# Optimization experiments

Hardware: AMD Instinct MI355X
Metric: run time of the kernel (lower is better)

The kernel has to match this reference:

```python
import jax, jax.numpy as jnp
from jax import lax
import numpy as np

B, N, P, NB = 64, 16, 20, 30      # frames, boxes/frame, num_persons, num_behaviors
C, F, OUT, SR = 1024, 14, 3, 2    # fmap channels, fmap size, roi output, sampling ratio
EPS = 1e-5


def roi_align_one(fmap, boxes):
    """fmap: [C,H,W]; boxes: [K,4]=(x1,y1,x2,y2) in fmap coords. Returns [K,C,OUT,OUT].
    torchvision-style roi_align (aligned=False) with fixed sampling_ratio=SR."""
    H, W = fmap.shape[1], fmap.shape[2]
    x1, y1, x2, y2 = boxes[:, 0], boxes[:, 1], boxes[:, 2], boxes[:, 3]
    rw = jnp.maximum(x2 - x1, 1.0)
    rh = jnp.maximum(y2 - y1, 1.0)
    S = OUT * SR
    pos = (jnp.arange(S, dtype=fmap.dtype) + 0.5) / SR            # sample pos in bin units
    ys = jnp.clip(y1[:, None] + pos[None, :] * (rh / OUT)[:, None], 0.0, H - 1.0)  # [K,S]
    xs = jnp.clip(x1[:, None] + pos[None, :] * (rw / OUT)[:, None], 0.0, W - 1.0)
    y0 = jnp.floor(ys); x0 = jnp.floor(xs)
    y0i = y0.astype(jnp.int32); x0i = x0.astype(jnp.int32)
    y1i = jnp.minimum(y0i + 1, H - 1); x1i = jnp.minimum(x0i + 1, W - 1)
    wy = ys - y0; wx = xs - x0                                     # [K,S]
    g = lambda yi, xi: fmap[:, yi[:, :, None], xi[:, None, :]]     # [C,K,S,S]
    v = (g(y0i, x0i) * ((1 - wy)[:, :, None] * (1 - wx)[:, None, :])
         + g(y0i, x1i) * ((1 - wy)[:, :, None] * wx[:, None, :])
         + g(y1i, x0i) * (wy[:, :, None] * (1 - wx)[:, None, :])
         + g(y1i, x1i) * (wy[:, :, None] * wx[:, None, :]))
    v = jnp.transpose(v, (1, 0, 2, 3))                             # [K,C,S,S]
    K = boxes.shape[0]
    return v.reshape(K, C, OUT, SR, OUT, SR).mean(axis=(3, 5))     # avg over samples


roi_align = jax.vmap(roi_align_one, in_axes=(0, 0))


def bn(x, g, b, m, v):
    s = (g / jnp.sqrt(v + EPS))[None, :, None, None]
    return x * s + (b - m * g / jnp.sqrt(v + EPS))[None, :, None, None]


def leaky(x):
    return jnp.where(x > 0, x, 0.1 * x)


def behavior_conv(x, w1, g1, b1, m1, v1, w2, g2, b2, m2, v2):
    dn = ('NCHW', 'OIHW', 'NCHW')
    x = lax.conv_general_dilated(x, w1, (1, 1), 'SAME', dimension_numbers=dn)
    x = leaky(bn(x, g1, b1, m1, v1))
    x = lax.conv_general_dilated(x, w2, (1, 1), 'SAME', dimension_numbers=dn)
    return leaky(bn(x, g2, b2, m2, v2))


def forward(fmap, boxes, conv1_w, bn1_g, bn1_b, bn1_m, bn1_v,
            conv2_w, bn2_g, bn2_b, bn2_m, bn2_v,
            conv1d_w, conv1d_b, fc1_w, fc1_b, fc2_w, fc2_b, person_idx):
    # --- global feature: ROI over the whole fmap per frame ---
    gbox = jnp.broadcast_to(jnp.array([[0.0, 0.0, F, F]], jnp.float32), (B, 1, 4))
    g_roi = roi_align(fmap, gbox).reshape(B, C, OUT, OUT)          # [B,1024,3,3]
    g_feat = behavior_conv(g_roi, conv1_w, bn1_g, bn1_b, bn1_m, bn1_v,
                           conv2_w, bn2_g, bn2_b, bn2_m, bn2_v)    # [B,256,3,3]
    g_feat = g_feat.reshape(B, 256 * OUT * OUT)                    # [B,2304]

    # --- per-box ROI features ---
    i_roi = roi_align(fmap, boxes).reshape(B * N, C, OUT, OUT)     # [B*N,1024,3,3]
    i_feat = behavior_conv(i_roi, conv1_w, bn1_g, bn1_b, bn1_m, bn1_v,
                           conv2_w, bn2_g, bn2_b, bn2_m, bn2_v)
    i_feat = i_feat.reshape(B, N, 256 * OUT * OUT)                 # [B,N,2304]

    # --- scatter-accumulate into behavior tensor [B,P,2304] ---
    behavior = jnp.broadcast_to(g_feat[:, None, :], (B, P, 2304))
    bidx = jnp.broadcast_to(jnp.arange(B)[:, None], (B, N))
    behavior = behavior.at[bidx, person_idx].add(i_feat)

    # --- temporal conv1d across the batch axis for every person slot ---
    x = jnp.transpose(behavior, (1, 2, 0))                         # [P,2304,B]
    x = lax.conv_general_dilated(x, conv1d_w, (1,), 'SAME',
                                 dimension_numbers=('NCH', 'OIH', 'NCH'))
    x = x + conv1d_b[None, :, None]                                # [P,2304,B]

    # --- gather each (frame, box)'s person feature at its frame and classify ---
    x = jnp.transpose(x, (2, 0, 1))                                # [B,P,2304]
    feats = jnp.take_along_axis(x, person_idx[:, :, None], axis=1) # [B,N,2304]
    h = jax.nn.relu(feats @ fc1_w + fc1_b)                         # dropout off (eval)
    return h @ fc2_w + fc2_b                                       # [B,N,NB]


def setup_inputs() -> dict:
    key = jax.random.key(0)
    ks = jax.random.split(key, 16)
    fmap = jax.random.normal(ks[0], (B, C, F, F), jnp.float32)
    lo = jax.random.uniform(ks[1], (B, N, 2), jnp.float32, 0.0, 9.0)
    sz = jax.random.uniform(ks[2], (B, N, 2), jnp.float32, 2.0, 5.0)
    hi = jnp.minimum(lo + sz, float(F))
    boxes = jnp.concatenate([lo, hi], axis=-1)                     # (x1,y1,x2,y2)
    person_idx = jax.random.randint(ks[3], (B, N), 0, P)
    s = lambda k, shape, fan: jax.random.normal(k, shape, jnp.float32) / np.sqrt(fan)
    return {
        'fmap': fmap, 'boxes': boxes, 'person_idx': person_idx,
        'conv1_w': s(ks[4], (512, 1024, 3, 3), 1024 * 9),
        'bn1_g': jnp.ones(512), 'bn1_b': jnp.zeros(512),
        'bn1_m': jnp.zeros(512), 'bn1_v': jnp.ones(512),
        'conv2_w': s(ks[5], (256, 512, 3, 3), 512 * 9),
        'bn2_g': jnp.ones(256), 'bn2_b': jnp.zeros(256),
        'bn2_m': jnp.zeros(256), 'bn2_v': jnp.ones(256),
        'conv1d_w': s(ks[6], (2304, 2304, 3), 2304 * 3),
        'conv1d_b': jnp.zeros(2304),
        'fc1_w': s(ks[7], (2304, 1024), 2304), 'fc1_b': jnp.zeros(1024),
        'fc2_w': s(ks[8], (1024, NB), 1024), 'fc2_b': jnp.zeros(NB),
    }


def reference(fmap, boxes, person_idx, conv1_w, bn1_g, bn1_b, bn1_m, bn1_v,
              conv2_w, bn2_g, bn2_b, bn2_m, bn2_v,
              conv1d_w, conv1d_b, fc1_w, fc1_b, fc2_w, fc2_b):
    return forward(fmap, boxes, conv1_w, bn1_g, bn1_b, bn1_m, bn1_v,
                   conv2_w, bn2_g, bn2_b, bn2_m, bn2_v,
                   conv1d_w, conv1d_b, fc1_w, fc1_b, fc2_w, fc2_b, person_idx)
```

## Files before the change

kernel.cpp:

```cpp
#include <hip/hip_runtime.h>
#include <hip/hip_bf16.h>
#include <cstdint>
#include <cstddef>

typedef __bf16 bf16;
typedef __bf16 bf16x8 __attribute__((ext_vector_type(8)));
typedef float f32x4 __attribute__((ext_vector_type(4)));

__device__ __forceinline__ void gload_lds16(const bf16* g, bf16* l) {
    __builtin_amdgcn_global_load_lds((const __attribute__((address_space(1))) void*)g,
                                     (__attribute__((address_space(3))) void*)l, 16, 0, 0);
}

template <int NT>
__global__ void __launch_bounds__(256) repack_w(const float* __restrict__ w, bf16* __restrict__ out,
                                                int OC, int IC) {
    int idx = blockIdx.x * 256 + threadIdx.x;
    if (idx >= OC * IC) return;
    int oc = idx / IC;
    int ic = idx - oc * IC;
    const float* src = w + (size_t)idx * NT;
    #pragma unroll
    for (int t = 0; t < NT; t++)
        out[(size_t)oc * NT * IC + t * IC + ic] = (bf16)src[t];
}

__global__ void __launch_bounds__(256) transpose_fc1(const float* __restrict__ w, bf16* __restrict__ out) {
    __shared__ float t[32][33];
    int iT = blockIdx.x * 32;
    int oT = blockIdx.y * 32;
    int tx = threadIdx.x, ty = threadIdx.y;
    #pragma unroll
    for (int j = 0; j < 4; j++)
        t[ty + j * 8][tx] = w[(size_t)(iT + ty + j * 8) * 1024 + oT + tx];
    __syncthreads();
    #pragma unroll
    for (int j = 0; j < 4; j++)
        out[(size_t)(oT + ty + j * 8) * 2304 + iT + tx] = (bf16)t[tx][ty + j * 8];
}

__global__ void __launch_bounds__(256) transpose_w2(const float* __restrict__ w, bf16* __restrict__ out) {
    int idx = blockIdx.x * 256 + threadIdx.x;
    if (idx >= 30 * 1024) return;
    int n = idx / 1024, k = idx - n * 1024;
    out[idx] = (bf16)w[(size_t)k * 30 + n];
}

__global__ void __launch_bounds__(256) setup_all(int* __restrict__ rb1t, int* __restrict__ rb2t,
                                                 int* __restrict__ rb1dt, int* __restrict__ rbfc,
                                                 const int* __restrict__ pidx,
                                                 bf16* __restrict__ zp1, bf16* __restrict__ zp2,
                                                 bf16* __restrict__ zp3,
                                                 const float* g1, const float* b1, const float* m1, const float* v1,
                                                 const float* g2, const float* b2, const float* m2, const float* v2,
                                                 float* __restrict__ s1, float* __restrict__ t1,
                                                 float* __restrict__ s2, float* __restrict__ t2) {
    int m = blockIdx.x * 256 + threadIdx.x;
    if (m < 9 * 9856) {
        int tap = m / 9856, r = m - tap * 9856;
        int mm = r < 9792 ? r : 0;
        int img = mm / 9, pos = mm - img * 9;
        int oy = pos / 3, ox = pos - oy * 3;
        int ty = tap / 3, tx = tap - ty * 3;
        int iy = oy + ty - 1, ix = ox + tx - 1;
        bool valid = (iy >= 0) & (iy < 3) & (ix >= 0) & (ix < 3);
        int cell = img * 9 + iy * 3 + ix;
        rb1t[m] = valid ? 1024 + cell * 1024 : 0;
        rb2t[m] = valid ? 512 + cell * 512 : 0;
    }
    if (m < 3 * 1280) {
        int tap = m / 1280, r = m - tap * 1280;
        int p = r >> 6, t = r & 63;
        int tt = t + tap - 1;
        bool valid = (tt >= 0) & (tt < 64);
        rb1dt[m] = valid ? 2304 + (p * 64 + tt) * 2304 : 0;
    }
    if (m < 1024) {
        int b = m >> 4;
        rbfc[m] = (b * 20 + pidx[m]) * 2304;
    }
    if (m < 1024) zp1[m] = (bf16)0.f;
    if (m < 512)  zp2[m] = (bf16)0.f;
    if (m < 2304) zp3[m] = (bf16)0.f;
    if (m < 512) {
        float sc = g1[m] * rsqrtf(v1[m] + 1e-5f);
        s1[m] = sc; t1[m] = b1[m] - m1[m] * sc;
    } else if (m < 768) {
        int i = m - 512;
        float sc = g2[i] * rsqrtf(v2[i] + 1e-5f);
        s2[i] = sc; t2[i] = b2[i] - m2[i] * sc;
    }
}

__global__ void __launch_bounds__(256) transpose_fmap(const float* __restrict__ fmap, bf16* __restrict__ fml) {
    __shared__ float t[32][33];
    int img = blockIdx.z;
    int hwT = blockIdx.x * 32;
    int cT  = blockIdx.y * 32;
    int tx = threadIdx.x, ty = threadIdx.y;
    #pragma unroll
    for (int j = 0; j < 4; j++) {
        int c = cT + ty + j * 8;
        int hw = hwT + tx;
        if (hw < 196)
            t[ty + j * 8][tx] = fmap[((size_t)img * 1024 + c) * 196 + hw];
    }
    __syncthreads();
    #pragma unroll
    for (int j = 0; j < 4; j++) {
        int hw = hwT + ty + j * 8;
        int c = cT + tx;
        if (hw < 196)
            fml[((size_t)img * 196 + hw) * 1024 + c] = (bf16)t[tx][ty + j * 8];
    }
}

__global__ void __launch_bounds__(128) roi_kernel2(const bf16* __restrict__ fml, const float* __restrict__ boxes,
                                                   bf16* __restrict__ a1c) {
    int box = blockIdx.x;
    int tid = threadIdx.x;
    float x1, y1, x2, y2;
    int img;
    if (box < 64) { img = box; x1 = 0.f; y1 = 0.f; x2 = 14.f; y2 = 14.f; }
    else {
        int ib = box - 64;
        img = ib >> 4;
        const float* bb = boxes + (size_t)ib * 4;
        x1 = bb[0]; y1 = bb[1]; x2 = bb[2]; y2 = bb[3];
    }
    float rw = fmaxf(x2 - x1, 1.f), rh = fmaxf(y2 - y1, 1.f);
    __shared__ float swy[6], swx[6];
    __shared__ int sy0[6], sx0[6];
    if (tid < 6) {
        int i = tid;
        float pos = ((float)i + 0.5f) * 0.5f;
        float yv = fminf(fmaxf(y1 + pos * (rh * (1.f / 3.f)), 0.f), 13.f);
        float y0 = floorf(yv);
        sy0[i] = (int)y0; swy[i] = yv - y0;
        float xv = fminf(fmaxf(x1 + pos * (rw * (1.f / 3.f)), 0.f), 13.f);
        float x0 = floorf(xv);
        sx0[i] = (int)x0; swx[i] = xv - x0;
    }
    __syncthreads();
    const bf16* base = fml + (size_t)img * 196 * 1024 + tid * 8;
    #pragma unroll
    for (int oy = 0; oy < 3; oy++) {
        #pragma unroll
        for (int ox = 0; ox < 3; ox++) {
            float acc[8];
            #pragma unroll
            for (int e = 0; e < 8; e++) acc[e] = 0.f;
            #pragma unroll
            for (int dy = 0; dy < 2; dy++) {
                int sy = 2 * oy + dy;
                int y0 = sy0[sy]; float wy = swy[sy];
                int y1i = min(y0 + 1, 13);
                #pragma unroll
                for (int dx = 0; dx < 2; dx++) {
                    int sx = 2 * ox + dx;
                    int x0 = sx0[sx]; float wx = swx[sx];
                    int x1i = min(x0 + 1, 13);
                    bf16x8 f00 = *(const bf16x8*)(base + (size_t)(y0 * 14 + x0) * 1024);
                    bf16x8 f01 = *(const bf16x8*)(base + (size_t)(y0 * 14 + x1i) * 1024);
                    bf16x8 f10 = *(const bf16x8*)(base + (size_t)(y1i * 14 + x0) * 1024);
                    bf16x8 f11 = *(const bf16x8*)(base + (size_t)(y1i * 14 + x1i) * 1024);
                    float w00 = (1.f - wy) * (1.f - wx), w01 = (1.f - wy) * wx;
                    float w10 = wy * (1.f - wx),         w11 = wy * wx;
                    #pragma unroll
                    for (int e = 0; e < 8; e++)
                        acc[e] += w00 * (float)f00[e] + w01 * (float)f01[e]
                                + w10 * (float)f10[e] + w11 * (float)f11[e];
                }
            }
            bf16x8 o;
            #pragma unroll
            for (int e = 0; e < 8; e++) o[e] = (bf16)(acc[e] * 0.25f);
            *(bf16x8*)(a1c + 1024 + ((size_t)box * 9 + oy * 3 + ox) * 1024 + tid * 8) = o;
        }
    }
}

__global__ void __launch_bounds__(256) assemble(const float* __restrict__ feat, const int* __restrict__ pidx,
                                                bf16* __restrict__ asm3) {
    int b = blockIdx.x;
    int p = blockIdx.y;
    __shared__ int idxs[16];
    if (threadIdx.x < 16) idxs[threadIdx.x] = pidx[b * 16 + threadIdx.x];
    __syncthreads();
    const float* g = feat + (size_t)b * 2304;
    for (int f = threadIdx.x; f < 2304; f += 256) {
        float v = g[f];
        #pragma unroll
        for (int n = 0; n < 16; n++)
            if (idxs[n] == p) v += feat[(size_t)(64 + b * 16 + n) * 2304 + f];
        asm3[2304 + ((size_t)p * 64 + b) * 2304 + f] = (bf16)v;
    }
}

template <int MODE, int NSPLIT>
__global__ void __launch_bounds__(256) gemm_k(const bf16* __restrict__ A, const int* __restrict__ rowtab,
                                              const bf16* __restrict__ Bw, float* __restrict__ outp) {
    constexpr int K   = MODE == 0 ? 9216 : MODE == 1 ? 4608 : MODE == 2 ? 6912 : 2304;
    constexpr int N   = MODE == 0 ? 512  : MODE == 1 ? 256  : MODE == 2 ? 2304 : 1024;
    constexpr int Cin = MODE == 0 ? 1024 : MODE == 1 ? 512  : 2304;
    constexpr int M   = MODE <= 1 ? 9792 : MODE == 2 ? 1280 : 1024;
    constexpr int MT  = MODE <= 1 ? 9856 : MODE == 2 ? 1280 : 1024;
    constexpr bool MPAD = (M % 128) != 0;
    constexpr int KTS = (K / 64) / NSPLIT;

    const int bm = blockIdx.y * 128;
    const int bn = blockIdx.x * 128;
    const int z  = blockIdx.z;
    const int tid = threadIdx.x;
    const int lane = tid & 63, wave = tid >> 6;
    const int q = lane >> 4, ln16 = lane & 15;
    const int wr = wave >> 1, wc = wave & 1;

    __shared__ __align__(16) bf16 As[128 * 64];
    __shared__ __align__(16) bf16 Bs[128 * 64];

    const int sr = lane >> 3;
    const int sc = ((lane & 7) ^ sr) * 8;
    const bf16* gB[4];
    #pragma unroll
    for (int u = 0; u < 4; u++)
        gB[u] = Bw + (size_t)(bn + wave * 32 + u * 8 + sr) * K + sc;

    f32x4 acc[4][4];
    #pragma unroll
    for (int mt = 0; mt < 4; mt++)
        #pragma unroll
        for (int nt = 0; nt < 4; nt++)
            acc[mt][nt] = (f32x4){0.f, 0.f, 0.f, 0.f};

    int rbA[4];
    int curtap = -1;
    for (int kt = z * KTS; kt < z * KTS + KTS; kt++) {
        const int k0 = kt * 64;
        const int tap = k0 / Cin;
        const int inner = k0 - tap * Cin;
        if (tap != curtap) {
            curtap = tap;
            #pragma unroll
            for (int u = 0; u < 4; u++)
                rbA[u] = rowtab[tap * MT + bm + wave * 32 + u * 8 + sr];
        }
        const int aoff = inner + sc;

        __syncthreads();
        #pragma unroll
        for (int u = 0; u < 4; u++)
            gload_lds16(A + (size_t)(rbA[u] + aoff), As + (wave * 32 + u * 8) * 64);
        #pragma unroll
        for (int u = 0; u < 4; u++)
            gload_lds16(gB[u] + k0, Bs + (wave * 32 + u * 8) * 64);
        __syncthreads();

        #pragma unroll
        for (int s = 0; s < 2; s++) {
            bf16x8 af[4], bfr[4];
            #pragma unroll
            for (int mt = 0; mt < 4; mt++) {
                int r = wr * 64 + mt * 16 + ln16;
                af[mt] = *(const bf16x8*)(As + r * 64 + (((4 * s + q) ^ (ln16 & 7)) << 3));
            }
            #pragma unroll
            for (int nt = 0; nt < 4; nt++) {
                int r = wc * 64 + nt * 16 + ln16;
                bfr[nt] = *(const bf16x8*)(Bs + r * 64 + (((4 * s + q) ^ (ln16 & 7)) << 3));
            }
            #pragma unroll
            for (int mt = 0; mt < 4; mt++)
                #pragma unroll
                for (int nt = 0; nt < 4; nt++)
                    acc[mt][nt] = __builtin_amdgcn_mfma_f32_16x16x32_bf16(af[mt], bfr[nt], acc[mt][nt], 0, 0, 0);
        }
    }

    #pragma unroll
    for (int mt = 0; mt < 4; mt++) {
        int gmBase = bm + wr * 64 + mt * 16 + q * 4;
        #pragma unroll
        for (int r = 0; r < 4; r++) {
            int gm = gmBase + r;
            if (MPAD && gm >= M) continue;
            #pragma unroll
            for (int nt = 0; nt < 4; nt++) {
                int gn = bn + wc * 64 + nt * 16 + ln16;
                outp[((size_t)z * M + gm) * N + gn] = acc[mt][nt][r];
            }
        }
    }
}

template <int RMODE>
__global__ void __launch_bounds__(256) reduce_k(const float* __restrict__ part, void* __restrict__ outp,
                                                const float* __restrict__ c0, const float* __restrict__ c1) {
    constexpr int M = RMODE == 0 ? 9792 : RMODE == 1 ? 1280 : RMODE == 2 ? 1024 : 9792;
    constexpr int N = RMODE == 0 ? 256  : RMODE == 1 ? 2304 : RMODE == 2 ? 1024 : 512;
    constexpr int S = RMODE == 0 ? 6    : RMODE == 1 ? 4    : RMODE == 2 ? 6    : 3;
    int idx = blockIdx.x * 256 + threadIdx.x;
    if (idx >= M * N) return;
    int m = idx / N, n = idx - m * N;
    float v = 0.f;
    #pragma unroll
    for (int s = 0; s < S; s++) v += part[(size_t)s * M * N + idx];
    if constexpr (RMODE == 0) {
        v = v * c0[n] + c1[n];
        v = v > 0.f ? v : 0.1f * v;
        int img = m / 9, pos = m - img * 9;
        ((float*)outp)[(size_t)img * 2304 + n * 9 + pos] = v;
    } else if constexpr (RMODE == 1) {
        v += c0[n];
        int p = m >> 6, t = m & 63;
        ((bf16*)outp)[((size_t)t * 20 + p) * 2304 + n] = (bf16)v;
    } else if constexpr (RMODE == 2) {
        v = fmaxf(v + c0[n], 0.f);
        ((bf16*)outp)[idx] = (bf16)v;
    } else {
        v = v * c0[n] + c1[n];
        v = v > 0.f ? v : 0.1f * v;
        ((bf16*)outp)[512 + (size_t)m * 512 + n] = (bf16)v;
    }
}

__global__ void __launch_bounds__(256) fc2_kernel(const bf16* __restrict__ h, const bf16* __restrict__ w2t,
                                                  const float* __restrict__ b2, float* __restrict__ out) {
    int tid = threadIdx.x;
    int m = blockIdx.x * 8 + (tid >> 5);
    int n = tid & 31;
    int n2 = n < 30 ? n : 29;
    const bf16* hr = h + (size_t)m * 1024;
    const bf16* wr = w2t + (size_t)n2 * 1024;
    float acc = 0.f;
    for (int k = 0; k < 1024; k += 8) {
        bf16x8 hv = *(const bf16x8*)(hr + k);
        bf16x8 wv = *(const bf16x8*)(wr + k);
        #pragma unroll
        for (int e = 0; e < 8; e++) acc += (float)hv[e] * (float)wv[e];
    }
    if (n < 30) out[(size_t)m * 30 + n] = acc + b2[n];
}

extern "C" void kernel_launch(void* const* d_in, const int* in_sizes, int n_in,
                              void* d_out, int out_size, void* d_ws, size_t ws_size,
                              hipStream_t stream) {
    const float* fmap     = (const float*)d_in[0];
    const float* boxes    = (const float*)d_in[1];
    const int*   pidx     = (const int*)d_in[2];
    const float* conv1_w  = (const float*)d_in[3];
    const float* bn1_g    = (const float*)d_in[4];
    const float* bn1_b    = (const float*)d_in[5];
    const float* bn1_m    = (const float*)d_in[6];
    const float* bn1_v    = (const float*)d_in[7];
    const float* conv2_w  = (const float*)d_in[8];
    const float* bn2_g    = (const float*)d_in[9];
    const float* bn2_b    = (const float*)d_in[10];
    const float* bn2_m    = (const float*)d_in[11];
    const float* bn2_v    = (const float*)d_in[12];
    const float* conv1d_w = (const float*)d_in[13];
    const float* conv1d_b = (const float*)d_in[14];
    const float* fc1_w    = (const float*)d_in[15];
    const float* fc1_b    = (const float*)d_in[16];
    const float* fc2_w    = (const float*)d_in[17];
    const float* fc2_b    = (const float*)d_in[18];
    float* out = (float*)d_out;

    char* ws = (char*)d_ws;

    float* s1    = (float*)(ws + 0);
    float* t1    = (float*)(ws + 2048);
    float* s2    = (float*)(ws + 4096);
    float* t2    = (float*)(ws + 5120);
    int*   rbfc  = (int*)(ws + 6144);
    int*   rb1dt = (int*)(ws + 10240);
    int*   rb1t  = (int*)(ws + 25600);
    int*   rb2t  = (int*)(ws + 380416);
    bf16*  fml    = (bf16*)(ws + 768000);
    float* part1  = (float*)(ws + 768000);
    float* part2  = (float*)(ws + 768000);
    float* part1d = (float*)(ws + 768000);
    float* partfc = (float*)(ws + 768000);
    bf16*  a1c    = (bf16*)(ws + 60930048);
    bf16*  wb1d   = (bf16*)(ws + 60930048);
    bf16*  fc1t   = (bf16*)(ws + 92780544);
    bf16*  xbuf   = (bf16*)(ws + 97499136);
    bf16*  hbuf   = (bf16*)(ws + 103397376);
    bf16*  w2t    = (bf16*)(ws + 105494528);
    bf16*  wb1    = (bf16*)(ws + 105555968);
    bf16*  wb2    = (bf16*)(ws + 114993152);
    bf16*  a2c    = (bf16*)(ws + 117352448);
    bf16*  asm3   = (bf16*)(ws + 127380480);
    float* feat   = (float*)(ws + 133283328);

    bf16* zp1 = a1c;
    bf16* zp2 = a2c;
    bf16* zp3 = asm3;

    setup_all<<<(9 * 9856 + 255) / 256, 256, 0, stream>>>(rb1t, rb2t, rb1dt, rbfc, pidx,
                                                          zp1, zp2, zp3,
                                                          bn1_g, bn1_b, bn1_m, bn1_v,
                                                          bn2_g, bn2_b, bn2_m, bn2_v,
                                                          s1, t1, s2, t2);
    repack_w<9><<<(512 * 1024 + 255) / 256, 256, 0, stream>>>(conv1_w, wb1, 512, 1024);
    repack_w<9><<<(256 * 512 + 255) / 256, 256, 0, stream>>>(conv2_w, wb2, 256, 512);

    transpose_fmap<<<dim3(7, 32, 64), dim3(32, 8), 0, stream>>>(fmap, fml);
    roi_kernel2<<<1088, 128, 0, stream>>>(fml, boxes, a1c);

    gemm_k<0, 3><<<dim3(4, 77, 3), 256, 0, stream>>>(a1c, rb1t, wb1, part1);
    reduce_k<3><<<(9792 * 512 + 255) / 256, 256, 0, stream>>>(part1, a2c, s1, t1);

    repack_w<3><<<(2304 * 2304 + 255) / 256, 256, 0, stream>>>(conv1d_w, wb1d, 2304, 2304);
    transpose_fc1<<<dim3(72, 32), dim3(32, 8), 0, stream>>>(fc1_w, fc1t);
    transpose_w2<<<(30 * 1024 + 255) / 256, 256, 0, stream>>>(fc2_w, w2t);

    gemm_k<1, 6><<<dim3(2, 77, 6), 256, 0, stream>>>(a2c, rb2t, wb2, part2);
    reduce_k<0><<<(9792 * 256 + 255) / 256, 256, 0, stream>>>(part2, feat, s2, t2);
    assemble<<<dim3(64, 20), 256, 0, stream>>>(feat, pidx, asm3);
    gemm_k<2, 4><<<dim3(18, 10, 4), 256, 0, stream>>>(asm3, rb1dt, wb1d, part1d);
    reduce_k<1><<<(1280 * 2304 + 255) / 256, 256, 0, stream>>>(part1d, xbuf, conv1d_b, nullptr);
    gemm_k<3, 6><<<dim3(8, 8, 6), 256, 0, stream>>>(xbuf, rbfc, fc1t, partfc);
    reduce_k<2><<<(1024 * 1024 + 255) / 256, 256, 0, stream>>>(partfc, hbuf, fc1_b, nullptr);
    fc2_kernel<<<128, 256, 0, stream>>>(hbuf, w2t, fc2_b, out);
    (void)in_sizes; (void)n_in; (void)out_size; (void)ws_size;
}
```

Baseline: 502.9 us.

## Compute conv1d only for gathered rows, tile conv2 reduce, fold fc2 transpose into setup

The conv1d GEMM now computes only the 1024 rows that the fc layer later gathers (frame, person_idx) rather than all 1280 person-time rows. Row tables are rebuilt to match, and fc1 reads the result with an identity table. The conv2 split-K reduce is replaced by a tiled kernel that transposes through shared memory, so the NCHW-flattened writes are coalesced. The fc2 weight transpose is merged into the setup kernel to save a launch. Together these reduce GEMM work, memory traffic and launch count.

```diff
diff --git a/kernel.cpp b/kernel.cpp
--- a/kernel.cpp
+++ b/kernel.cpp
@@ -39,22 +39,16 @@
         out[(size_t)(oT + ty + j * 8) * 2304 + iT + tx] = (bf16)t[tx][ty + j * 8];
 }
 
-__global__ void __launch_bounds__(256) transpose_w2(const float* __restrict__ w, bf16* __restrict__ out) {
-    int idx = blockIdx.x * 256 + threadIdx.x;
-    if (idx >= 30 * 1024) return;
-    int n = idx / 1024, k = idx - n * 1024;
-    out[idx] = (bf16)w[(size_t)k * 30 + n];
-}
-
 __global__ void __launch_bounds__(256) setup_all(int* __restrict__ rb1t, int* __restrict__ rb2t,
-                                                 int* __restrict__ rb1dt, int* __restrict__ rbfc,
+                                                 int* __restrict__ rb1dg, int* __restrict__ rbid,
                                                  const int* __restrict__ pidx,
                                                  bf16* __restrict__ zp1, bf16* __restrict__ zp2,
                                                  bf16* __restrict__ zp3,
                                                  const float* g1, const float* b1, const float* m1, const float* v1,
                                                  const float* g2, const float* b2, const float* m2, const float* v2,
                                                  float* __restrict__ s1, float* __restrict__ t1,
-                                                 float* __restrict__ s2, float* __restrict__ t2) {
+                                                 float* __restrict__ s2, float* __restrict__ t2,
+                                                 const float* __restrict__ fc2_w, bf16* __restrict__ w2t) {
     int m = blockIdx.x * 256 + threadIdx.x;
     if (m < 9 * 9856) {
         int tap = m / 9856, r = m - tap * 9856;
@@ -68,16 +62,18 @@
         rb1t[m] = valid ? 1024 + cell * 1024 : 0;
         rb2t[m] = valid ? 512 + cell * 512 : 0;
     }
-    if (m < 3 * 1280) {
-        int tap = m / 1280, r = m - tap * 1280;
-        int p = r >> 6, t = r & 63;
-        int tt = t + tap - 1;
+    if (m < 3 * 1024) {
+        int tap = m / 1024, r = m - tap * 1024;
+        int b = r >> 4;
+        int p = pidx[r];
+        int tt = b + tap - 1;
         bool valid = (tt >= 0) & (tt < 64);
-        rb1dt[m] = valid ? 2304 + (p * 64 + tt) * 2304 : 0;
-    }
-    if (m < 1024) {
-        int b = m >> 4;
-        rbfc[m] = (b * 20 + pidx[m]) * 2304;
+        rb1dg[m] = valid ? 2304 + (p * 64 + tt) * 2304 : 0;
+    }
+    if (m < 1024) rbid[m] = m * 2304;
+    if (m < 30 * 1024) {
+        int n = m / 1024, k = m - n * 1024;
+        w2t[m] = (bf16)fc2_w[(size_t)k * 30 + n];
     }
     if (m < 1024) zp1[m] = (bf16)0.f;
     if (m < 512)  zp2[m] = (bf16)0.f;
@@ -203,8 +199,8 @@
     constexpr int K   = MODE == 0 ? 9216 : MODE == 1 ? 4608 : MODE == 2 ? 6912 : 2304;
     constexpr int N   = MODE == 0 ? 512  : MODE == 1 ? 256  : MODE == 2 ? 2304 : 1024;
     constexpr int Cin = MODE == 0 ? 1024 : MODE == 1 ? 512  : 2304;
-    constexpr int M   = MODE <= 1 ? 9792 : MODE == 2 ? 1280 : 1024;
-    constexpr int MT  = MODE <= 1 ? 9856 : MODE == 2 ? 1280 : 1024;
+    constexpr int M   = MODE <= 1 ? 9792 : 1024;
+    constexpr int MT  = MODE <= 1 ? 9856 : 1024;
     constexpr bool MPAD = (M % 128) != 0;
     constexpr int KTS = (K / 64) / NSPLIT;
 
@@ -293,27 +289,53 @@
     }
 }
 
+__global__ void __launch_bounds__(256) reduce0_tiled(const float* __restrict__ part,
+                                                     float* __restrict__ feat,
+                                                     const float* __restrict__ s2, const float* __restrict__ t2) {
+    int c = blockIdx.x;
+    int t = threadIdx.x;
+    float acc[9];
+    #pragma unroll
+    for (int r = 0; r < 9; r++) acc[r] = 0.f;
+    #pragma unroll
+    for (int z = 0; z < 6; z++) {
+        const float* base = part + ((size_t)z * 9792 + c * 9) * 256 + t;
+        #pragma unroll
+        for (int r = 0; r < 9; r++) acc[r] += base[r * 256];
+    }
+    float s = s2[t], b = t2[t];
+    __shared__ float L[9 * 257];
+    #pragma unroll
+    for (int r = 0; r < 9; r++) {
+        float v = acc[r] * s + b;
+        v = v > 0.f ? v : 0.1f * v;
+        L[r * 257 + t] = v;
+    }
+    __syncthreads();
+    float* fout = feat + (size_t)c * 2304;
+    #pragma unroll
+    for (int k = 0; k < 9; k++) {
+        int f = t + k * 256;
+        int oc = f / 9, pos = f - oc * 9;
+        fout[f] = L[pos * 257 + oc];
+    }
+}
+
 template <int RMODE>
 __global__ void __launch_bounds__(256) reduce_k(const float* __restrict__ part, void* __restrict__ outp,
                                                 const float* __restrict__ c0, const float* __restrict__ c1) {
-    constexpr int M = RMODE == 0 ? 9792 : RMODE == 1 ? 1280 : RMODE == 2 ? 1024 : 9792;
-    constexpr int N = RMODE == 0 ? 256  : RMODE == 1 ? 2304 : RMODE == 2 ? 1024 : 512;
-    constexpr int S = RMODE == 0 ? 6    : RMODE == 1 ? 4    : RMODE == 2 ? 6    : 3;
+    constexpr int M = RMODE == 1 ? 1024 : RMODE == 2 ? 1024 : 9792;
+    constexpr int N = RMODE == 1 ? 2304 : RMODE == 2 ? 1024 : 512;
+    constexpr int S = RMODE == 1 ? 4    : RMODE == 2 ? 6    : 3;
     int idx = blockIdx.x * 256 + threadIdx.x;
     if (idx >= M * N) return;
     int m = idx / N, n = idx - m * N;
     float v = 0.f;
     #pragma unroll
     for (int s = 0; s < S; s++) v += part[(size_t)s * M * N + idx];
-    if constexpr (RMODE == 0) {
-        v = v * c0[n] + c1[n];
-        v = v > 0.f ? v : 0.1f * v;
-        int img = m / 9, pos = m - img * 9;
-        ((float*)outp)[(size_t)img * 2304 + n * 9 + pos] = v;
-    } else if constexpr (RMODE == 1) {
+    if constexpr (RMODE == 1) {
         v += c0[n];
-        int p = m >> 6, t = m & 63;
-        ((bf16*)outp)[((size_t)t * 20 + p) * 2304 + n] = (bf16)v;
+        ((bf16*)outp)[idx] = (bf16)v;
     } else if constexpr (RMODE == 2) {
         v = fmaxf(v + c0[n], 0.f);
         ((bf16*)outp)[idx] = (bf16)v;
@@ -372,8 +394,8 @@
     float* t1    = (float*)(ws + 2048);
     float* s2    = (float*)(ws + 4096);
     float* t2    = (float*)(ws + 5120);
-    int*   rbfc  = (int*)(ws + 6144);
-    int*   rb1dt = (int*)(ws + 10240);
+    int*   rbid  = (int*)(ws + 6144);
+    int*   rb1dg = (int*)(ws + 10240);
     int*   rb1t  = (int*)(ws + 25600);
     int*   rb2t  = (int*)(ws + 380416);
     bf16*  fml    = (bf16*)(ws + 768000);
@@ -385,23 +407,23 @@
     bf16*  wb1d   = (bf16*)(ws + 60930048);
     bf16*  fc1t   = (bf16*)(ws + 92780544);
     bf16*  xbuf   = (bf16*)(ws + 97499136);
-    bf16*  hbuf   = (bf16*)(ws + 103397376);
-    bf16*  w2t    = (bf16*)(ws + 105494528);
-    bf16*  wb1    = (bf16*)(ws + 105555968);
-    bf16*  wb2    = (bf16*)(ws + 114993152);
-    bf16*  a2c    = (bf16*)(ws + 117352448);
-    bf16*  asm3   = (bf16*)(ws + 127380480);
-    float* feat   = (float*)(ws + 133283328);
+    bf16*  hbuf   = (bf16*)(ws + 102217728);
+    bf16*  w2t    = (bf16*)(ws + 104314880);
+    bf16*  wb1    = (bf16*)(ws + 104857600);
+    bf16*  wb2    = (bf16*)(ws + 114294784);
+    bf16*  a2c    = (bf16*)(ws + 116654080);
+    bf16*  asm3   = (bf16*)(ws + 126682112);
+    float* feat   = (float*)(ws + 132584960);
 
     bf16* zp1 = a1c;
     bf16* zp2 = a2c;
     bf16* zp3 = asm3;
 
-    setup_all<<<(9 * 9856 + 255) / 256, 256, 0, stream>>>(rb1t, rb2t, rb1dt, rbfc, pidx,
+    setup_all<<<(9 * 9856 + 255) / 256, 256, 0, stream>>>(rb1t, rb2t, rb1dg, rbid, pidx,
                                                           zp1, zp2, zp3,
                                                           bn1_g, bn1_b, bn1_m, bn1_v,
                                                           bn2_g, bn2_b, bn2_m, bn2_v,
-                                                          s1, t1, s2, t2);
+                                                          s1, t1, s2, t2, fc2_w, w2t);
     repack_w<9><<<(512 * 1024 + 255) / 256, 256, 0, stream>>>(conv1_w, wb1, 512, 1024);
     repack_w<9><<<(256 * 512 + 255) / 256, 256, 0, stream>>>(conv2_w, wb2, 256, 512);
 
@@ -413,14 +435,13 @@
 
     repack_w<3><<<(2304 * 2304 + 255) / 256, 256, 0, stream>>>(conv1d_w, wb1d, 2304, 2304);
     transpose_fc1<<<dim3(72, 32), dim3(32, 8), 0, stream>>>(fc1_w, fc1t);
-    transpose_w2<<<(30 * 1024 + 255) / 256, 256, 0, stream>>>(fc2_w, w2t);
 
     gemm_k<1, 6><<<dim3(2, 77, 6), 256, 0, stream>>>(a2c, rb2t, wb2, part2);
-    reduce_k<0><<<(9792 * 256 + 255) / 256, 256, 0, stream>>>(part2, feat, s2, t2);
+    reduce0_tiled<<<1088, 256, 0, stream>>>(part2, feat, s2, t2);
     assemble<<<dim3(64, 20), 256, 0, stream>>>(feat, pidx, asm3);
-    gemm_k<2, 4><<<dim3(18, 10, 4), 256, 0, stream>>>(asm3, rb1dt, wb1d, part1d);
-    reduce_k<1><<<(1280 * 2304 + 255) / 256, 256, 0, stream>>>(part1d, xbuf, conv1d_b, nullptr);
-    gemm_k<3, 6><<<dim3(8, 8, 6), 256, 0, stream>>>(xbuf, rbfc, fc1t, partfc);
+    gemm_k<2, 4><<<dim3(18, 8, 4), 256, 0, stream>>>(asm3, rb1dg, wb1d, part1d);
+    reduce_k<1><<<(1024 * 2304 + 255) / 256, 256, 0, stream>>>(part1d, xbuf, conv1d_b, nullptr);
+    gemm_k<3, 6><<<dim3(8, 8, 6), 256, 0, stream>>>(xbuf, rbid, fc1t, partfc);
     reduce_k<2><<<(1024 * 1024 + 255) / 256, 256, 0, stream>>>(partfc, hbuf, fc1_b, nullptr);
     fc2_kernel<<<128, 256, 0, stream>>>(hbuf, w2t, fc2_b, out);
     (void)in_sizes; (void)n_in; (void)out_size; (void)ws_size;
```

After: 483.6 us. -3.8%, faster.
